# Optimization experiments

Hardware: AMD Instinct MI355X
Metric: run time of the kernel (lower is better)

Reference implementation:

```python
import jax, jax.numpy as jnp
import numpy as np

N_NODES = 100000
N_EDGES = 1600000
F_IN = 64
HID = 128
N_CLASSES = 16
N_GRAPHS = 128


def _glorot(key, shape):
    fan_in = shape[1]
    bound = 1.0 / np.sqrt(fan_in)
    return jax.random.uniform(key, shape, jnp.float32, -bound, bound)


def setup_inputs() -> dict:
    key = jax.random.key(0)
    ks = jax.random.split(key, 12)
    x = jax.random.normal(ks[0], (N_NODES, F_IN), jnp.float32)
    edge_index = jax.random.randint(ks[1], (2, N_EDGES), 0, N_NODES, jnp.int64)
    batch = jnp.sort(jax.random.randint(ks[2], (N_NODES,), 0, N_GRAPHS, jnp.int64))
    # GraphConv l: out = lin_rel(sum_j x_j) + lin_root(x); lin_rel has bias, lin_root does not.
    W1_rel = _glorot(ks[3], (HID, F_IN)); b1 = jnp.zeros((HID,), jnp.float32)
    W1_root = _glorot(ks[4], (HID, F_IN))
    W2_rel = _glorot(ks[5], (HID, HID)); b2 = jnp.zeros((HID,), jnp.float32)
    W2_root = _glorot(ks[6], (HID, HID))
    W3_rel = _glorot(ks[7], (HID, HID)); b3 = jnp.zeros((HID,), jnp.float32)
    W3_root = _glorot(ks[8], (HID, HID))
    W_lin = _glorot(ks[9], (N_CLASSES, HID))
    b_lin = jnp.zeros((N_CLASSES,), jnp.float32)
    return {"x": x, "edge_index": edge_index, "batch": batch,
            "W1_rel": W1_rel, "b1": b1, "W1_root": W1_root,
            "W2_rel": W2_rel, "b2": b2, "W2_root": W2_root,
            "W3_rel": W3_rel, "b3": b3, "W3_root": W3_root,
            "W_lin": W_lin, "b_lin": b_lin}


def graph_conv(x, src, dst, W_rel, b_rel, W_root):
    # gather messages from source nodes, scatter-add at targets
    agg = jax.ops.segment_sum(x[src], dst, num_segments=N_NODES)  # [N, in]
    return agg @ W_rel.T + b_rel + x @ W_root.T


def reference(x, edge_index, batch, W1_rel, b1, W1_root, W2_rel, b2, W2_root,
              W3_rel, b3, W3_root, W_lin, b_lin):
    src, dst = edge_index[0], edge_index[1]
    h = jax.nn.relu(graph_conv(x, src, dst, W1_rel, b1, W1_root))
    h = jax.nn.relu(graph_conv(h, src, dst, W2_rel, b2, W2_root))
    h = graph_conv(h, src, dst, W3_rel, b3, W3_root)
    # global_mean_pool over batch ids
    sums = jax.ops.segment_sum(h, batch, num_segments=N_GRAPHS)  # [G, HID]
    counts = jax.ops.segment_sum(jnp.ones((h.shape[0],), h.dtype), batch,
                                 num_segments=N_GRAPHS)
    pooled = sums / jnp.maximum(counts, 1.0)[:, None]
    # dropout is identity in eval mode
    return pooled @ W_lin.T + b_lin
```

## Files before the change

### kernel.cpp

```cpp
#include <hip/hip_runtime.h>

#define N_NODES_C 100000
#define N_GRAPHS_C 128

__global__ void hist_kernel(const int* __restrict__ ei, int E, int* __restrict__ deg) {
    int i = blockIdx.x * blockDim.x + threadIdx.x;
    if (i < E) atomicAdd(&deg[ei[E + i]], 1);
}

__global__ void scan1_kernel(const int* __restrict__ deg, int N,
                             int* __restrict__ tmp, int* __restrict__ bsum) {
    __shared__ int sh[512];
    int t = threadIdx.x;
    int i = blockIdx.x * 512 + t;
    int v = (i < N) ? deg[i] : 0;
    sh[t] = v;
    __syncthreads();
    for (int off = 1; off < 512; off <<= 1) {
        int add = (t >= off) ? sh[t - off] : 0;
        __syncthreads();
        sh[t] += add;
        __syncthreads();
    }
    if (i < N) tmp[i] = sh[t] - v;
    if (t == 511) bsum[blockIdx.x] = sh[511];
}

__global__ void scan2_kernel(int* bsum, int nb) {
    if (threadIdx.x == 0 && blockIdx.x == 0) {
        int run = 0;
        for (int j = 0; j < nb; ++j) { int v = bsum[j]; bsum[j] = run; run += v; }
    }
}

__global__ void scan3_kernel(const int* __restrict__ tmp, const int* __restrict__ bsum,
                             int N, int* __restrict__ rowp) {
    int i = blockIdx.x * 512 + threadIdx.x;
    if (i < N) rowp[i] = tmp[i] + bsum[blockIdx.x];
}

__global__ void fill_kernel(const int* __restrict__ ei, int E, const int* __restrict__ rowp,
                            int* __restrict__ cursor, int* __restrict__ csr) {
    int i = blockIdx.x * blockDim.x + threadIdx.x;
    if (i < E) {
        int d = ei[E + i];
        int pos = rowp[d] + atomicAdd(&cursor[d], 1);
        csr[pos] = ei[i];
    }
}

template <int FIN>
__global__ __launch_bounds__(256) void agg_kernel(const float* __restrict__ xin,
                                                  const int* __restrict__ rowp,
                                                  const int* __restrict__ degv,
                                                  const int* __restrict__ csrc,
                                                  float* __restrict__ aggout, int nNodes) {
    int wave = blockIdx.x * 4 + (threadIdx.x >> 6);
    int lane = threadIdx.x & 63;
    if (wave >= nNodes) return;
    int start = rowp[wave];
    int deg = degv[wave];

    float s0 = 0.f, s1 = 0.f, s2 = 0.f, s3 = 0.f;
    float2 a0 = {0.f,0.f}, a1 = {0.f,0.f}, a2 = {0.f,0.f}, a3 = {0.f,0.f};
    const float2* xin2 = (const float2*)xin;

    for (int base = 0; base < deg; base += 64) {
        int cnt = min(64, deg - base);
        int sid = (lane < cnt) ? csrc[start + base + lane] : 0;
        int j = 0;
        for (; j + 4 <= cnt; j += 4) {
            int n0 = __shfl(sid, j + 0);
            int n1 = __shfl(sid, j + 1);
            int n2 = __shfl(sid, j + 2);
            int n3 = __shfl(sid, j + 3);
            if (FIN == 64) {
                float v0 = xin[n0 * 64 + lane];
                float v1 = xin[n1 * 64 + lane];
                float v2 = xin[n2 * 64 + lane];
                float v3 = xin[n3 * 64 + lane];
                s0 += v0; s1 += v1; s2 += v2; s3 += v3;
            } else {
                float2 v0 = xin2[n0 * 64 + lane];
                float2 v1 = xin2[n1 * 64 + lane];
                float2 v2 = xin2[n2 * 64 + lane];
                float2 v3 = xin2[n3 * 64 + lane];
                a0.x += v0.x; a0.y += v0.y;
                a1.x += v1.x; a1.y += v1.y;
                a2.x += v2.x; a2.y += v2.y;
                a3.x += v3.x; a3.y += v3.y;
            }
        }
        for (; j < cnt; ++j) {
            int s = __shfl(sid, j);
            if (FIN == 64) {
                s0 += xin[s * 64 + lane];
            } else {
                float2 v = xin2[s * 64 + lane];
                a0.x += v.x; a0.y += v.y;
            }
        }
    }
    if (FIN == 64) {
        aggout[wave * 64 + lane] = (s0 + s1) + (s2 + s3);
    } else {
        float2 o;
        o.x = (a0.x + a1.x) + (a2.x + a3.x);
        o.y = (a0.y + a1.y) + (a2.y + a3.y);
        ((float2*)aggout)[wave * 64 + lane] = o;
    }
}

template <int KTOT, bool RELU>
__global__ __launch_bounds__(256) void xform_kernel(
    const float* __restrict__ agg, const float* __restrict__ xin,
    const float* __restrict__ Wrel, const float* __restrict__ Wroot,
    const float* __restrict__ bias, float* __restrict__ hout, int nNodes)
{
    constexpr int KH = KTOT / 2;
    constexpr int NC = KTOT / 16;
    __shared__ float sA[2][16][128];
    __shared__ float sW[2][16][128];
    const int t  = threadIdx.x;
    const int nb0 = blockIdx.x * 128;
    const int tx = t & 15;
    const int ty = t >> 4;
    const int ln = t & 127;
    const int lj = t >> 7;

    float acc[8][8];
#pragma unroll
    for (int r = 0; r < 8; ++r)
#pragma unroll
        for (int c = 0; c < 8; ++c) acc[r][c] = 0.f;

    const int gn = nb0 + ln;
    const bool gvalid = gn < nNodes;
    const size_t arow = (size_t)gn * KH;

    float4 va[2], vw[2];
    auto loadChunk = [&](int cix) {
        int kc = cix * 16;
        const float* srcA = (kc < KH) ? agg : xin;
        const float* srcW = (kc < KH) ? Wrel : Wroot;
        int kof = (kc < KH) ? kc : kc - KH;
#pragma unroll
        for (int q = 0; q < 2; ++q) {
            int j = lj + q * 2;
            va[q] = gvalid ? *(const float4*)&srcA[arow + kof + j * 4]
                           : make_float4(0.f, 0.f, 0.f, 0.f);
            vw[q] = *(const float4*)&srcW[(size_t)ln * KH + kof + j * 4];
        }
    };
    auto writeChunk = [&](int buf) {
#pragma unroll
        for (int q = 0; q < 2; ++q) {
            int j = lj + q * 2;
            sA[buf][j * 4 + 0][ln] = va[q].x; sA[buf][j * 4 + 1][ln] = va[q].y;
            sA[buf][j * 4 + 2][ln] = va[q].z; sA[buf][j * 4 + 3][ln] = va[q].w;
            sW[buf][j * 4 + 0][ln] = vw[q].x; sW[buf][j * 4 + 1][ln] = vw[q].y;
            sW[buf][j * 4 + 2][ln] = vw[q].z; sW[buf][j * 4 + 3][ln] = vw[q].w;
        }
    };

    loadChunk(0);
    writeChunk(0);
    if (NC > 1) loadChunk(1);
    __syncthreads();

#pragma unroll 1
    for (int cix = 0; cix < NC; ++cix) {
        const int cur = cix & 1;
        if (cix + 1 < NC) {
            writeChunk(cur ^ 1);
            if (cix + 2 < NC) loadChunk(cix + 2);
        }
#pragma unroll
        for (int i = 0; i < 16; ++i) {
            float4 a0 = *(const float4*)&sA[cur][i][tx * 4];
            float4 a1 = *(const float4*)&sA[cur][i][64 + tx * 4];
            float4 w0 = *(const float4*)&sW[cur][i][ty * 4];
            float4 w1 = *(const float4*)&sW[cur][i][64 + ty * 4];
            float av[8] = {a0.x, a0.y, a0.z, a0.w, a1.x, a1.y, a1.z, a1.w};
            float wv[8] = {w0.x, w0.y, w0.z, w0.w, w1.x, w1.y, w1.z, w1.w};
#pragma unroll
            for (int r = 0; r < 8; ++r)
#pragma unroll
                for (int c = 0; c < 8; ++c)
                    acc[r][c] += av[r] * wv[c];
        }
        __syncthreads();
    }

    float4 b0 = *(const float4*)&bias[ty * 4];
    float4 b1 = *(const float4*)&bias[64 + ty * 4];
    float bv[8] = {b0.x, b0.y, b0.z, b0.w, b1.x, b1.y, b1.z, b1.w};
#pragma unroll
    for (int r = 0; r < 8; ++r) {
        int n = nb0 + ((r < 4) ? (tx * 4 + r) : (64 + tx * 4 + (r - 4)));
        if (n >= nNodes) continue;
        float4 o0, o1;
        o0.x = acc[r][0] + bv[0]; o0.y = acc[r][1] + bv[1];
        o0.z = acc[r][2] + bv[2]; o0.w = acc[r][3] + bv[3];
        o1.x = acc[r][4] + bv[4]; o1.y = acc[r][5] + bv[5];
        o1.z = acc[r][6] + bv[6]; o1.w = acc[r][7] + bv[7];
        if (RELU) {
            o0.x = fmaxf(o0.x, 0.f); o0.y = fmaxf(o0.y, 0.f);
            o0.z = fmaxf(o0.z, 0.f); o0.w = fmaxf(o0.w, 0.f);
            o1.x = fmaxf(o1.x, 0.f); o1.y = fmaxf(o1.y, 0.f);
            o1.z = fmaxf(o1.z, 0.f); o1.w = fmaxf(o1.w, 0.f);
        }
        *(float4*)&hout[(size_t)n * 128 + ty * 4] = o0;
        *(float4*)&hout[(size_t)n * 128 + 64 + ty * 4] = o1;
    }
}

__global__ void bounds_kernel(const int* __restrict__ batch, int N, int* __restrict__ gstart) {
    int g = blockIdx.x * blockDim.x + threadIdx.x;
    if (g > N_GRAPHS_C) return;
    int lo = 0, hi = N;
    while (lo < hi) {
        int mid = (lo + hi) >> 1;
        if (batch[mid] < g) lo = mid + 1; else hi = mid;
    }
    gstart[g] = lo;
}

__global__ __launch_bounds__(256) void pool2_kernel(const float* __restrict__ h,
                                                    const int* __restrict__ gstart,
                                                    float* __restrict__ pooled) {
    int g = blockIdx.x;
    int f = threadIdx.x & 127;
    int sub = threadIdx.x >> 7;
    int s = gstart[g], e = gstart[g + 1];
    float acc = 0.f;
    for (int n = s + sub; n < e; n += 2) acc += h[(size_t)n * 128 + f];
    __shared__ float sh[128];
    if (sub == 1) sh[f] = acc;
    __syncthreads();
    if (sub == 0) {
        float tot = acc + sh[f];
        float inv = 1.0f / fmaxf((float)(e - s), 1.0f);
        pooled[g * 128 + f] = tot * inv;
    }
}

__global__ void final_kernel(const float* __restrict__ pooled,
                             const float* __restrict__ Wlin, const float* __restrict__ blin,
                             float* __restrict__ out) {
    int idx = blockIdx.x * blockDim.x + threadIdx.x;
    int g = idx >> 4, c = idx & 15;
    float s = 0.f;
    for (int k = 0; k < 128; ++k) s += pooled[g * 128 + k] * Wlin[c * 128 + k];
    out[idx] = s + blin[c];
}

extern "C" void kernel_launch(void* const* d_in, const int* in_sizes, int n_in,
                              void* d_out, int out_size, void* d_ws, size_t ws_size,
                              hipStream_t stream) {
    const float* x      = (const float*)d_in[0];
    const int*   ei     = (const int*)d_in[1];
    const int*   batch  = (const int*)d_in[2];
    const float* W1_rel = (const float*)d_in[3];
    const float* b1     = (const float*)d_in[4];
    const float* W1_root= (const float*)d_in[5];
    const float* W2_rel = (const float*)d_in[6];
    const float* b2     = (const float*)d_in[7];
    const float* W2_root= (const float*)d_in[8];
    const float* W3_rel = (const float*)d_in[9];
    const float* b3     = (const float*)d_in[10];
    const float* W3_root= (const float*)d_in[11];
    const float* W_lin  = (const float*)d_in[12];
    const float* b_lin  = (const float*)d_in[13];
    float* out = (float*)d_out;

    const int N = in_sizes[2];
    const int E = in_sizes[1] / 2;
    const int nb = (N + 511) / 512;

    char* base = (char*)d_ws;
    size_t off = 0;
    auto carve = [&](size_t bytes) -> void* {
        void* p = base + off;
        off = (off + bytes + 255) & ~(size_t)255;
        return p;
    };
    int*   deg    = (int*)carve((size_t)N * 4);
    int*   tmp    = (int*)carve((size_t)N * 4);
    int*   bsum   = (int*)carve(1024);
    int*   rowp   = (int*)carve((size_t)(N + 1) * 4);
    int*   cursor = (int*)carve((size_t)N * 4);
    int*   csr    = (int*)carve((size_t)E * 4);
    float* aggbuf = (float*)carve((size_t)N * 128 * 4);
    float* hA     = (float*)carve((size_t)N * 128 * 4);
    float* hB     = (float*)carve((size_t)N * 128 * 4);
    float* pooled = (float*)carve((size_t)N_GRAPHS_C * 128 * 4);
    int*   gstart = (int*)carve((size_t)(N_GRAPHS_C + 1) * 4);
    (void)ws_size;

    hipMemsetAsync(deg, 0, (size_t)N * 4, stream);
    hipMemsetAsync(cursor, 0, (size_t)N * 4, stream);

    hist_kernel<<<(E + 255) / 256, 256, 0, stream>>>(ei, E, deg);
    scan1_kernel<<<nb, 512, 0, stream>>>(deg, N, tmp, bsum);
    scan2_kernel<<<1, 64, 0, stream>>>(bsum, nb);
    scan3_kernel<<<nb, 512, 0, stream>>>(tmp, bsum, N, rowp);
    fill_kernel<<<(E + 255) / 256, 256, 0, stream>>>(ei, E, rowp, cursor, csr);

    bounds_kernel<<<1, 192, 0, stream>>>(batch, N, gstart);

    const int aggGrid = (N + 3) / 4;
    const int xGrid = (N + 127) / 128;

    agg_kernel<64><<<aggGrid, 256, 0, stream>>>(x, rowp, deg, csr, aggbuf, N);
    xform_kernel<128, true><<<xGrid, 256, 0, stream>>>(
        aggbuf, x, W1_rel, W1_root, b1, hA, N);

    agg_kernel<128><<<aggGrid, 256, 0, stream>>>(hA, rowp, deg, csr, aggbuf, N);
    xform_kernel<256, true><<<xGrid, 256, 0, stream>>>(
        aggbuf, hA, W2_rel, W2_root, b2, hB, N);

    agg_kernel<128><<<aggGrid, 256, 0, stream>>>(hB, rowp, deg, csr, aggbuf, N);
    xform_kernel<256, false><<<xGrid, 256, 0, stream>>>(
        aggbuf, hB, W3_rel, W3_root, b3, hA, N);

    pool2_kernel<<<N_GRAPHS_C, 256, 0, stream>>>(hA, gstart, pooled);
    final_kernel<<<8, 256, 0, stream>>>(pooled, W_lin, b_lin, out);
}
```

Before: 910.7 us.

## Use split-bf16 MFMA for node transforms and widen gather unroll to eight

The FP32 FMA tile GEMM in xform_kernel is replaced with bf16 MFMA 16x16x32 instructions. Each fp32 value is split into a high and a low bf16 part, and three MFMA products (hh, hl, lh) recover near-fp32 accuracy. A new wprep kernel pre-packs the weights into a swizzled bf16 hi/lo image to avoid LDS bank conflicts. The aggregation gather loop is unrolled to eight independent accumulators for more memory-level parallelism. The cost is three extra small kernel launches and a slight accuracy loss from dropping the low*low term.

```diff
diff --git a/kernel.cpp b/kernel.cpp
--- a/kernel.cpp
+++ b/kernel.cpp
@@ -2,6 +2,13 @@
 
 #define N_NODES_C 100000
 #define N_GRAPHS_C 128
+
+typedef __attribute__((ext_vector_type(8))) __bf16 bf16x8;
+typedef __attribute__((ext_vector_type(4))) float f32x4;
+
+__device__ __forceinline__ f32x4 mfma16(bf16x8 a, bf16x8 b, f32x4 c) {
+    return __builtin_amdgcn_mfma_f32_16x16x32_bf16(a, b, c, 0, 0, 0);
+}
 
 __global__ void hist_kernel(const int* __restrict__ ei, int E, int* __restrict__ deg) {
     int i = blockIdx.x * blockDim.x + threadIdx.x;
@@ -60,108 +67,167 @@
     if (wave >= nNodes) return;
     int start = rowp[wave];
     int deg = degv[wave];
-
-    float s0 = 0.f, s1 = 0.f, s2 = 0.f, s3 = 0.f;
-    float2 a0 = {0.f,0.f}, a1 = {0.f,0.f}, a2 = {0.f,0.f}, a3 = {0.f,0.f};
     const float2* xin2 = (const float2*)xin;
 
-    for (int base = 0; base < deg; base += 64) {
-        int cnt = min(64, deg - base);
-        int sid = (lane < cnt) ? csrc[start + base + lane] : 0;
-        int j = 0;
-        for (; j + 4 <= cnt; j += 4) {
-            int n0 = __shfl(sid, j + 0);
-            int n1 = __shfl(sid, j + 1);
-            int n2 = __shfl(sid, j + 2);
-            int n3 = __shfl(sid, j + 3);
-            if (FIN == 64) {
-                float v0 = xin[n0 * 64 + lane];
-                float v1 = xin[n1 * 64 + lane];
-                float v2 = xin[n2 * 64 + lane];
-                float v3 = xin[n3 * 64 + lane];
-                s0 += v0; s1 += v1; s2 += v2; s3 += v3;
-            } else {
-                float2 v0 = xin2[n0 * 64 + lane];
-                float2 v1 = xin2[n1 * 64 + lane];
-                float2 v2 = xin2[n2 * 64 + lane];
-                float2 v3 = xin2[n3 * 64 + lane];
-                a0.x += v0.x; a0.y += v0.y;
-                a1.x += v1.x; a1.y += v1.y;
-                a2.x += v2.x; a2.y += v2.y;
-                a3.x += v3.x; a3.y += v3.y;
-            }
-        }
-        for (; j < cnt; ++j) {
-            int s = __shfl(sid, j);
-            if (FIN == 64) {
-                s0 += xin[s * 64 + lane];
-            } else {
-                float2 v = xin2[s * 64 + lane];
-                a0.x += v.x; a0.y += v.y;
-            }
-        }
-    }
     if (FIN == 64) {
-        aggout[wave * 64 + lane] = (s0 + s1) + (s2 + s3);
+        float s[8];
+#pragma unroll
+        for (int q = 0; q < 8; ++q) s[q] = 0.f;
+        for (int base = 0; base < deg; base += 64) {
+            int cnt = min(64, deg - base);
+            int sid = (lane < cnt) ? csrc[start + base + lane] : 0;
+            int j = 0;
+            for (; j + 8 <= cnt; j += 8) {
+                int n[8];
+#pragma unroll
+                for (int q = 0; q < 8; ++q) n[q] = __shfl(sid, j + q);
+#pragma unroll
+                for (int q = 0; q < 8; ++q) s[q] += xin[n[q] * 64 + lane];
+            }
+            for (; j < cnt; ++j) s[0] += xin[__shfl(sid, j) * 64 + lane];
+        }
+        aggout[wave * 64 + lane] = ((s[0]+s[1])+(s[2]+s[3])) + ((s[4]+s[5])+(s[6]+s[7]));
     } else {
+        float2 a[8];
+#pragma unroll
+        for (int q = 0; q < 8; ++q) { a[q].x = 0.f; a[q].y = 0.f; }
+        for (int base = 0; base < deg; base += 64) {
+            int cnt = min(64, deg - base);
+            int sid = (lane < cnt) ? csrc[start + base + lane] : 0;
+            int j = 0;
+            for (; j + 8 <= cnt; j += 8) {
+                int n[8];
+#pragma unroll
+                for (int q = 0; q < 8; ++q) n[q] = __shfl(sid, j + q);
+#pragma unroll
+                for (int q = 0; q < 8; ++q) {
+                    float2 v = xin2[n[q] * 64 + lane];
+                    a[q].x += v.x; a[q].y += v.y;
+                }
+            }
+            for (; j < cnt; ++j) {
+                float2 v = xin2[__shfl(sid, j) * 64 + lane];
+                a[0].x += v.x; a[0].y += v.y;
+            }
+        }
         float2 o;
-        o.x = (a0.x + a1.x) + (a2.x + a3.x);
-        o.y = (a0.y + a1.y) + (a2.y + a3.y);
+        o.x = ((a[0].x+a[1].x)+(a[2].x+a[3].x)) + ((a[4].x+a[5].x)+(a[6].x+a[7].x));
+        o.y = ((a[0].y+a[1].y)+(a[2].y+a[3].y)) + ((a[4].y+a[5].y)+(a[6].y+a[7].y));
         ((float2*)aggout)[wave * 64 + lane] = o;
     }
 }
 
+__global__ void wprep_kernel(const float* __restrict__ Wrel, const float* __restrict__ Wroot,
+                             int KH, unsigned* __restrict__ img) {
+    int cid = blockIdx.x;
+    int col = threadIdx.x;
+    int key = (col >> 1) & 3;
+    unsigned hiw[16], low[16];
+#pragma unroll 4
+    for (int p = 0; p < 16; ++p) {
+        int k0 = cid * 32 + p * 2;
+        float v0 = (k0 < KH) ? Wrel[col * KH + k0] : Wroot[col * KH + k0 - KH];
+        float v1 = (k0 + 1 < KH) ? Wrel[col * KH + k0 + 1] : Wroot[col * KH + k0 + 1 - KH];
+        unsigned u0 = __float_as_uint(v0), u1 = __float_as_uint(v1);
+        unsigned h0 = u0 & 0xFFFF0000u, h1 = u1 & 0xFFFF0000u;
+        float l0 = v0 - __uint_as_float(h0), l1 = v1 - __uint_as_float(h1);
+        unsigned lb0 = __float_as_uint(l0) & 0xFFFF0000u;
+        unsigned lb1 = __float_as_uint(l1) & 0xFFFF0000u;
+        hiw[p] = (h0 >> 16) | h1;
+        low[p] = (lb0 >> 16) | lb1;
+    }
+    unsigned* cb = img + (size_t)cid * 4096;
+#pragma unroll 4
+    for (int p = 0; p < 16; ++p) {
+        int s = p >> 2, w = p & 3;
+        int sp = s ^ key;
+        cb[col * 16 + sp * 4 + w] = hiw[p];
+        cb[2048 + col * 16 + sp * 4 + w] = low[p];
+    }
+}
+
 template <int KTOT, bool RELU>
-__global__ __launch_bounds__(256) void xform_kernel(
+__global__ __launch_bounds__(256, 2) void xform_kernel(
     const float* __restrict__ agg, const float* __restrict__ xin,
-    const float* __restrict__ Wrel, const float* __restrict__ Wroot,
-    const float* __restrict__ bias, float* __restrict__ hout, int nNodes)
+    const unsigned* __restrict__ wimg, const float* __restrict__ bias,
+    float* __restrict__ hout, int nNodes)
 {
     constexpr int KH = KTOT / 2;
-    constexpr int NC = KTOT / 16;
-    __shared__ float sA[2][16][128];
-    __shared__ float sW[2][16][128];
-    const int t  = threadIdx.x;
+    constexpr int NC = KTOT / 32;
+    __shared__ unsigned sA[2][4096];
+    __shared__ unsigned sW[2][4096];
+    const int t = threadIdx.x;
     const int nb0 = blockIdx.x * 128;
-    const int tx = t & 15;
-    const int ty = t >> 4;
-    const int ln = t & 127;
-    const int lj = t >> 7;
-
-    float acc[8][8];
-#pragma unroll
-    for (int r = 0; r < 8; ++r)
-#pragma unroll
-        for (int c = 0; c < 8; ++c) acc[r][c] = 0.f;
-
-    const int gn = nb0 + ln;
+
+    const int srow = t >> 1;
+    const int skh = t & 1;
+    const int skey = (srow >> 1) & 3;
+    const int gn = nb0 + srow;
     const bool gvalid = gn < nNodes;
     const size_t arow = (size_t)gn * KH;
 
-    float4 va[2], vw[2];
+    float4 va[4]; uint4 vw[4];
     auto loadChunk = [&](int cix) {
-        int kc = cix * 16;
+        int kc = cix * 32 + skh * 16;
         const float* srcA = (kc < KH) ? agg : xin;
-        const float* srcW = (kc < KH) ? Wrel : Wroot;
         int kof = (kc < KH) ? kc : kc - KH;
-#pragma unroll
-        for (int q = 0; q < 2; ++q) {
-            int j = lj + q * 2;
-            va[q] = gvalid ? *(const float4*)&srcA[arow + kof + j * 4]
-                           : make_float4(0.f, 0.f, 0.f, 0.f);
-            vw[q] = *(const float4*)&srcW[(size_t)ln * KH + kof + j * 4];
-        }
+        if (gvalid) {
+#pragma unroll
+            for (int q = 0; q < 4; ++q)
+                va[q] = *(const float4*)&srcA[arow + kof + q * 4];
+        } else {
+#pragma unroll
+            for (int q = 0; q < 4; ++q) va[q] = make_float4(0.f, 0.f, 0.f, 0.f);
+        }
+        const uint4* wsrc = (const uint4*)(wimg + (size_t)cix * 4096) + t * 4;
+#pragma unroll
+        for (int q = 0; q < 4; ++q) vw[q] = wsrc[q];
     };
     auto writeChunk = [&](int buf) {
-#pragma unroll
-        for (int q = 0; q < 2; ++q) {
-            int j = lj + q * 2;
-            sA[buf][j * 4 + 0][ln] = va[q].x; sA[buf][j * 4 + 1][ln] = va[q].y;
-            sA[buf][j * 4 + 2][ln] = va[q].z; sA[buf][j * 4 + 3][ln] = va[q].w;
-            sW[buf][j * 4 + 0][ln] = vw[q].x; sW[buf][j * 4 + 1][ln] = vw[q].y;
-            sW[buf][j * 4 + 2][ln] = vw[q].z; sW[buf][j * 4 + 3][ln] = vw[q].w;
-        }
+        uint4* wd = (uint4*)&sW[buf][t * 16];
+#pragma unroll
+        for (int q = 0; q < 4; ++q) wd[q] = vw[q];
+        unsigned hiw[8], low[8];
+#pragma unroll
+        for (int q = 0; q < 4; ++q) {
+            float vv[4] = {va[q].x, va[q].y, va[q].z, va[q].w};
+#pragma unroll
+            for (int h = 0; h < 2; ++h) {
+                unsigned u0 = __float_as_uint(vv[h * 2]), u1 = __float_as_uint(vv[h * 2 + 1]);
+                unsigned h0 = u0 & 0xFFFF0000u, h1 = u1 & 0xFFFF0000u;
+                float l0 = vv[h * 2] - __uint_as_float(h0);
+                float l1 = vv[h * 2 + 1] - __uint_as_float(h1);
+                unsigned lb0 = __float_as_uint(l0) & 0xFFFF0000u;
+                unsigned lb1 = __float_as_uint(l1) & 0xFFFF0000u;
+                hiw[q * 2 + h] = (h0 >> 16) | h1;
+                low[q * 2 + h] = (lb0 >> 16) | lb1;
+            }
+        }
+        int s0 = (skh * 2) ^ skey, s1 = (skh * 2 + 1) ^ skey;
+        unsigned* abH = &sA[buf][srow * 16];
+        unsigned* abL = &sA[buf][2048 + srow * 16];
+        *(uint4*)&abH[s0 * 4] = make_uint4(hiw[0], hiw[1], hiw[2], hiw[3]);
+        *(uint4*)&abH[s1 * 4] = make_uint4(hiw[4], hiw[5], hiw[6], hiw[7]);
+        *(uint4*)&abL[s0 * 4] = make_uint4(low[0], low[1], low[2], low[3]);
+        *(uint4*)&abL[s1 * 4] = make_uint4(low[4], low[5], low[6], low[7]);
     };
+
+    const int lane = t & 63, wv = t >> 6;
+    const int r15 = lane & 15, hi4 = lane >> 4;
+    const int ckey = (r15 >> 1) & 3;
+    const int cslot = (hi4 ^ ckey) * 4;
+    const int arow0 = (wv * 32 + r15) * 16;
+    const int arow1 = arow0 + 256;
+
+    f32x4 acc[2][8];
+#pragma unroll
+    for (int g = 0; g < 2; ++g)
+#pragma unroll
+        for (int j = 0; j < 8; ++j) acc[g][j] = (f32x4){0.f, 0.f, 0.f, 0.f};
+
+    float bj[8];
+#pragma unroll
+    for (int j = 0; j < 8; ++j) bj[j] = bias[j * 16 + r15];
 
     loadChunk(0);
     writeChunk(0);
@@ -175,43 +241,41 @@
             writeChunk(cur ^ 1);
             if (cix + 2 < NC) loadChunk(cix + 2);
         }
-#pragma unroll
-        for (int i = 0; i < 16; ++i) {
-            float4 a0 = *(const float4*)&sA[cur][i][tx * 4];
-            float4 a1 = *(const float4*)&sA[cur][i][64 + tx * 4];
-            float4 w0 = *(const float4*)&sW[cur][i][ty * 4];
-            float4 w1 = *(const float4*)&sW[cur][i][64 + ty * 4];
-            float av[8] = {a0.x, a0.y, a0.z, a0.w, a1.x, a1.y, a1.z, a1.w};
-            float wv[8] = {w0.x, w0.y, w0.z, w0.w, w1.x, w1.y, w1.z, w1.w};
-#pragma unroll
-            for (int r = 0; r < 8; ++r)
-#pragma unroll
-                for (int c = 0; c < 8; ++c)
-                    acc[r][c] += av[r] * wv[c];
+        const unsigned* A = sA[cur];
+        const unsigned* W = sW[cur];
+        bf16x8 ah0 = *(const bf16x8*)&A[arow0 + cslot];
+        bf16x8 ah1 = *(const bf16x8*)&A[arow1 + cslot];
+        bf16x8 al0 = *(const bf16x8*)&A[2048 + arow0 + cslot];
+        bf16x8 al1 = *(const bf16x8*)&A[2048 + arow1 + cslot];
+#pragma unroll
+        for (int j = 0; j < 8; ++j) {
+            int cb = (j * 16 + r15) * 16;
+            bf16x8 bh = *(const bf16x8*)&W[cb + cslot];
+            bf16x8 bl = *(const bf16x8*)&W[2048 + cb + cslot];
+            acc[0][j] = mfma16(ah0, bh, acc[0][j]);
+            acc[1][j] = mfma16(ah1, bh, acc[1][j]);
+            acc[0][j] = mfma16(ah0, bl, acc[0][j]);
+            acc[1][j] = mfma16(ah1, bl, acc[1][j]);
+            acc[0][j] = mfma16(al0, bh, acc[0][j]);
+            acc[1][j] = mfma16(al1, bh, acc[1][j]);
         }
         __syncthreads();
     }
 
-    float4 b0 = *(const float4*)&bias[ty * 4];
-    float4 b1 = *(const float4*)&bias[64 + ty * 4];
-    float bv[8] = {b0.x, b0.y, b0.z, b0.w, b1.x, b1.y, b1.z, b1.w};
-#pragma unroll
-    for (int r = 0; r < 8; ++r) {
-        int n = nb0 + ((r < 4) ? (tx * 4 + r) : (64 + tx * 4 + (r - 4)));
-        if (n >= nNodes) continue;
-        float4 o0, o1;
-        o0.x = acc[r][0] + bv[0]; o0.y = acc[r][1] + bv[1];
-        o0.z = acc[r][2] + bv[2]; o0.w = acc[r][3] + bv[3];
-        o1.x = acc[r][4] + bv[4]; o1.y = acc[r][5] + bv[5];
-        o1.z = acc[r][6] + bv[6]; o1.w = acc[r][7] + bv[7];
-        if (RELU) {
-            o0.x = fmaxf(o0.x, 0.f); o0.y = fmaxf(o0.y, 0.f);
-            o0.z = fmaxf(o0.z, 0.f); o0.w = fmaxf(o0.w, 0.f);
-            o1.x = fmaxf(o1.x, 0.f); o1.y = fmaxf(o1.y, 0.f);
-            o1.z = fmaxf(o1.z, 0.f); o1.w = fmaxf(o1.w, 0.f);
-        }
-        *(float4*)&hout[(size_t)n * 128 + ty * 4] = o0;
-        *(float4*)&hout[(size_t)n * 128 + 64 + ty * 4] = o1;
+#pragma unroll
+    for (int g2 = 0; g2 < 2; ++g2) {
+#pragma unroll
+        for (int r = 0; r < 4; ++r) {
+            int node = nb0 + wv * 32 + g2 * 16 + hi4 * 4 + r;
+            if (node >= nNodes) continue;
+            float* orow = &hout[(size_t)node * 128];
+#pragma unroll
+            for (int j = 0; j < 8; ++j) {
+                float v = acc[g2][j][r] + bj[j];
+                if (RELU) v = fmaxf(v, 0.f);
+                orow[j * 16 + r15] = v;
+            }
+        }
     }
 }
 
@@ -285,21 +349,28 @@
         off = (off + bytes + 255) & ~(size_t)255;
         return p;
     };
-    int*   deg    = (int*)carve((size_t)N * 4);
-    int*   tmp    = (int*)carve((size_t)N * 4);
-    int*   bsum   = (int*)carve(1024);
-    int*   rowp   = (int*)carve((size_t)(N + 1) * 4);
-    int*   cursor = (int*)carve((size_t)N * 4);
-    int*   csr    = (int*)carve((size_t)E * 4);
-    float* aggbuf = (float*)carve((size_t)N * 128 * 4);
-    float* hA     = (float*)carve((size_t)N * 128 * 4);
-    float* hB     = (float*)carve((size_t)N * 128 * 4);
-    float* pooled = (float*)carve((size_t)N_GRAPHS_C * 128 * 4);
-    int*   gstart = (int*)carve((size_t)(N_GRAPHS_C + 1) * 4);
+    int*      deg    = (int*)carve((size_t)N * 4);
+    int*      tmp    = (int*)carve((size_t)N * 4);
+    int*      bsum   = (int*)carve(1024);
+    int*      rowp   = (int*)carve((size_t)(N + 1) * 4);
+    int*      cursor = (int*)carve((size_t)N * 4);
+    int*      csr    = (int*)carve((size_t)E * 4);
+    float*    aggbuf = (float*)carve((size_t)N * 128 * 4);
+    float*    hA     = (float*)carve((size_t)N * 128 * 4);
+    float*    hB     = (float*)carve((size_t)N * 128 * 4);
+    float*    pooled = (float*)carve((size_t)N_GRAPHS_C * 128 * 4);
+    int*      gstart = (int*)carve((size_t)(N_GRAPHS_C + 1) * 4);
+    unsigned* wimg1  = (unsigned*)carve((size_t)4 * 4096 * 4);
+    unsigned* wimg2  = (unsigned*)carve((size_t)8 * 4096 * 4);
+    unsigned* wimg3  = (unsigned*)carve((size_t)8 * 4096 * 4);
     (void)ws_size;
 
     hipMemsetAsync(deg, 0, (size_t)N * 4, stream);
     hipMemsetAsync(cursor, 0, (size_t)N * 4, stream);
+
+    wprep_kernel<<<4, 128, 0, stream>>>(W1_rel, W1_root, 64, wimg1);
+    wprep_kernel<<<8, 128, 0, stream>>>(W2_rel, W2_root, 128, wimg2);
+    wprep_kernel<<<8, 128, 0, stream>>>(W3_rel, W3_root, 128, wimg3);
 
     hist_kernel<<<(E + 255) / 256, 256, 0, stream>>>(ei, E, deg);
     scan1_kernel<<<nb, 512, 0, stream>>>(deg, N, tmp, bsum);
@@ -313,16 +384,13 @@
     const int xGrid = (N + 127) / 128;
 
     agg_kernel<64><<<aggGrid, 256, 0, stream>>>(x, rowp, deg, csr, aggbuf, N);
-    xform_kernel<128, true><<<xGrid, 256, 0, stream>>>(
-        aggbuf, x, W1_rel, W1_root, b1, hA, N);
+    xform_kernel<128, true><<<xGrid, 256, 0, stream>>>(aggbuf, x, wimg1, b1, hA, N);
 
     agg_kernel<128><<<aggGrid, 256, 0, stream>>>(hA, rowp, deg, csr, aggbuf, N);
-    xform_kernel<256, true><<<xGrid, 256, 0, stream>>>(
-        aggbuf, hA, W2_rel, W2_root, b2, hB, N);
+    xform_kernel<256, true><<<xGrid, 256, 0, stream>>>(aggbuf, hA, wimg2, b2, hB, N);
 
     agg_kernel<128><<<aggGrid, 256, 0, stream>>>(hB, rowp, deg, csr, aggbuf, N);
-    xform_kernel<256, false><<<xGrid, 256, 0, stream>>>(
-        aggbuf, hB, W3_rel, W3_root, b3, hA, N);
+    xform_kernel<256, false><<<xGrid, 256, 0, stream>>>(aggbuf, hB, wimg3, b3, hA, N);
 
     pool2_kernel<<<N_GRAPHS_C, 256, 0, stream>>>(hA, gstart, pooled);
     final_kernel<<<8, 256, 0, stream>>>(pooled, W_lin, b_lin, out);
```

Result: faster. 827.3 us (-9.2%).
